# Performance work log

Hardware: AMD Instinct MI355X
Metric: run time of the kernel (lower is better)

The kernel has to match this reference:

```python
import jax, jax.numpy as jnp
import numpy as np

VOCAB, EMBED, HID, MAXLEN, BATCH = 32000, 512, 512, 64, 32
DEC_H = 2 * HID  # decoder hidden width = 2*hidden_size


def _lstm_cell(x, h, c, wx, wh, b):
    # PyTorch LSTMCell gate order: i, f, g, o
    gates = x @ wx + h @ wh + b
    i, f, g, o = jnp.split(gates, 4, axis=-1)
    c = jax.nn.sigmoid(f) * c + jax.nn.sigmoid(i) * jnp.tanh(g)
    h = jax.nn.sigmoid(o) * jnp.tanh(c)
    return h, c


def setup_inputs() -> dict:
    key = jax.random.key(0)
    ks = jax.random.split(key, 12)
    s = 0.02
    inp = {
        "x": jax.random.randint(ks[0], (BATCH, MAXLEN), 0, VOCAB),
        # encoder: embedding [V, E], LSTM cell E -> 2H
        "enc_embed": jax.random.normal(ks[1], (VOCAB, EMBED), jnp.float32) * s,
        "enc_wx": jax.random.normal(ks[2], (EMBED, 4 * DEC_H), jnp.float32) * s,
        "enc_wh": jax.random.normal(ks[3], (DEC_H, 4 * DEC_H), jnp.float32) * s,
        "enc_b": jnp.zeros((4 * DEC_H,), jnp.float32),
        # decoder: embedding [V, 2H], Bahdanau attn, combine, LSTM cell 2H -> 2H, out proj
        "dec_embed": jax.random.normal(ks[4], (VOCAB, DEC_H), jnp.float32) * s,
        "attn_w": jax.random.normal(ks[5], (2 * DEC_H, MAXLEN), jnp.float32) * s,
        "attn_b": jnp.zeros((MAXLEN,), jnp.float32),
        "comb_w": jax.random.normal(ks[6], (2 * DEC_H, DEC_H), jnp.float32) * s,
        "comb_b": jnp.zeros((DEC_H,), jnp.float32),
        "dec_wx": jax.random.normal(ks[7], (DEC_H, 4 * DEC_H), jnp.float32) * s,
        "dec_wh": jax.random.normal(ks[8], (DEC_H, 4 * DEC_H), jnp.float32) * s,
        "dec_b": jnp.zeros((4 * DEC_H,), jnp.float32),
        "out_w": jax.random.normal(ks[9], (DEC_H, VOCAB), jnp.float32) * s,
        "out_b": jnp.zeros((VOCAB,), jnp.float32),
    }
    return inp


def reference(x, enc_embed, enc_wx, enc_wh, enc_b, dec_embed, attn_w, attn_b,
              comb_w, comb_b, dec_wx, dec_wh, dec_b, out_w, out_b):
    B = x.shape[0]

    # ---- encoder: one token per step, scan over time ----
    def enc_step(carry, tok):
        h, c = carry
        e = enc_embed[tok]  # (B, E)
        h, c = _lstm_cell(e, h, c, enc_wx, enc_wh, enc_b)
        return (h, c), h

    h0 = jnp.zeros((B, DEC_H), jnp.float32)
    (_, _), enc_outs = jax.lax.scan(enc_step, (h0, h0), x.T)  # (L, B, 2H)
    enc_outs = enc_outs.transpose(1, 0, 2)  # (B, L, 2H)

    # ---- decoder: Bahdanau attention + greedy feedback, scan over steps ----
    def dec_step(carry, _):
        h, c, tok = carry
        e = dec_embed[tok]  # (B, 2H)
        aw = jax.nn.softmax(jnp.concatenate([e, h], -1) @ attn_w + attn_b, -1)  # (B, L)
        ctx = jnp.einsum('bl,bld->bd', aw, enc_outs)  # (B, 2H)
        inp = jax.nn.relu(jnp.concatenate([e, ctx], -1) @ comb_w + comb_b)
        h, c = _lstm_cell(inp, h, c, dec_wx, dec_wh, dec_b)
        logp = jax.nn.log_softmax(h @ out_w + out_b, -1)  # (B, V)
        tok = jnp.argmax(logp, -1)
        return (h, c, tok), logp

    tok0 = jnp.full((B,), 127, dtype=x.dtype)
    (_, _, _), outs = jax.lax.scan(dec_step, (h0, h0, tok0), None, length=MAXLEN)
    return outs.transpose(1, 0, 2)  # (B, L, V)
```

## Files before the change

kernel.cpp:

```cpp
#include <hip/hip_runtime.h>

#define B   32
#define L   64
#define DH  1024
#define G4  4096
#define EK  512
#define V   32000

__device__ __forceinline__ float sigm(float x){ return 1.f/(1.f+expf(-x)); }
__device__ __forceinline__ unsigned mono(float f){
  unsigned u = __float_as_uint(f);
  return (u & 0x80000000u) ? ~u : (u | 0x80000000u);
}

__global__ __launch_bounds__(256) void init_kernel(float* h, float* c){
  int i = blockIdx.x*256 + threadIdx.x;
  if (i < B*DH){ h[i]=0.f; c[i]=0.f; }
}

__global__ __launch_bounds__(256) void gates_kernel(
    int mode, int t,
    const int* __restrict__ x, const float* __restrict__ embed,
    const float* __restrict__ src1, int K1,
    const float* __restrict__ wx, const float* __restrict__ wh,
    const float* __restrict__ bias,
    const float* __restrict__ h_in, float* __restrict__ h_out,
    float* __restrict__ cst, float* __restrict__ enc_outs)
{
  __shared__ float es[128][36];
  __shared__ int tok_s[B];
  __shared__ float gate_s[4][8][B];
  int tid = threadIdx.x;
  int hc = tid & 7, g = (tid>>3)&3, rg = tid>>5;
  int jh = blockIdx.x*8 + hc;
  int jg = g*DH + jh;
  float a0=0.f,a1=0.f,a2=0.f,a3=0.f;
  if (mode==0 && tid < B) tok_s[tid] = x[tid*L + t];
  __syncthreads();
  for (int phase=0; phase<2; ++phase){
    int K = phase ? DH : K1;
    const float* W = phase ? wh : wx;
    for (int kb=0; kb<K; kb+=128){
      for (int i=0;i<16;++i){
        int idx = i*256 + tid;
        int b = idx >> 7, kk = idx & 127;
        int k = kb + kk;
        float v;
        if (phase)          v = h_in[b*DH + k];
        else if (mode==0)   v = embed[(long)tok_s[b]*EK + k];
        else { v = src1[b*DH + k]; v = v>0.f ? v : 0.f; }
        es[kk][b] = v;
      }
      __syncthreads();
      #pragma unroll 8
      for (int kk=0; kk<128; ++kk){
        float w = W[(long)(kb+kk)*G4 + jg];
        float4 hv = *reinterpret_cast<const float4*>(&es[kk][rg*4]);
        a0 += hv.x*w; a1 += hv.y*w; a2 += hv.z*w; a3 += hv.w*w;
      }
      __syncthreads();
    }
  }
  float bj = bias[jg];
  gate_s[g][hc][rg*4+0] = a0+bj;
  gate_s[g][hc][rg*4+1] = a1+bj;
  gate_s[g][hc][rg*4+2] = a2+bj;
  gate_s[g][hc][rg*4+3] = a3+bj;
  __syncthreads();
  if (tid < 64){
    int hc2 = tid & 7, rg2 = tid >> 3;
    int j = blockIdx.x*8 + hc2;
    for (int i=0;i<4;++i){
      int b = rg2*4 + i;
      float iv = gate_s[0][hc2][b];
      float fv = gate_s[1][hc2][b];
      float gv = gate_s[2][hc2][b];
      float ov = gate_s[3][hc2][b];
      float cn = sigm(fv)*cst[b*DH + j] + sigm(iv)*tanhf(gv);
      cst[b*DH + j] = cn;
      float hv = sigm(ov)*tanhf(cn);
      h_out[b*DH + j] = hv;
      if (enc_outs) enc_outs[((long)b*L + t)*DH + j] = hv;
    }
  }
}

__global__ __launch_bounds__(256) void attn_kernel(
    int t, const unsigned long long* __restrict__ ptok,
    const float* __restrict__ dec_embed, const float* __restrict__ attn_w,
    const float* __restrict__ attn_b, const float* __restrict__ h_in,
    const float* __restrict__ enc_outs,
    float* __restrict__ e_buf, float* __restrict__ ctx,
    float* __restrict__ inp, const float* __restrict__ comb_b)
{
  __shared__ float e_s[DH], h_s[DH], sc_s[4][64], aw_s[64];
  __shared__ int tok_sh;
  int b = blockIdx.x, tid = threadIdx.x;
  if (tid==0){
    int tok = 127;
    if (t > 0) tok = (int)(~(unsigned)(ptok[(t-1)*B + b] & 0xffffffffull));
    tok_sh = tok;
  }
  __syncthreads();
  int tok = tok_sh;
  for (int i=0;i<4;++i){
    int k = i*256 + tid;
    float ev = dec_embed[(long)tok*DH + k];
    float hv = h_in[b*DH + k];
    e_s[k]=ev; h_s[k]=hv;
    e_buf[b*DH + k] = ev;
    inp[b*DH + k] = comb_b[k];
  }
  __syncthreads();
  int l = tid & 63, ks = tid >> 6;
  float p = 0.f;
  for (int kk=0; kk<512; ++kk){
    int k = ks*512 + kk;
    float sv = (k < DH) ? e_s[k] : h_s[k-DH];
    p += sv * attn_w[(long)k*64 + l];
  }
  sc_s[ks][l] = p;
  __syncthreads();
  if (tid < 64){
    float s = sc_s[0][l]+sc_s[1][l]+sc_s[2][l]+sc_s[3][l] + attn_b[l];
    float m = s;
    for (int off=32; off; off>>=1) m = fmaxf(m, __shfl_xor(m, off));
    float e = expf(s-m);
    float sum = e;
    for (int off=32; off; off>>=1) sum += __shfl_xor(sum, off);
    aw_s[l] = e/sum;
  }
  __syncthreads();
  float c0=0.f,c1=0.f,c2=0.f,c3=0.f;
  for (int ll=0; ll<64; ++ll){
    float a = aw_s[ll];
    const float* er = &enc_outs[((long)b*L + ll)*DH];
    c0 += a*er[tid]; c1 += a*er[256+tid]; c2 += a*er[512+tid]; c3 += a*er[768+tid];
  }
  ctx[b*DH + tid]       = c0;
  ctx[b*DH + 256 + tid] = c1;
  ctx[b*DH + 512 + tid] = c2;
  ctx[b*DH + 768 + tid] = c3;
}

__global__ __launch_bounds__(256) void comb_kernel(
    const float* __restrict__ e_buf, const float* __restrict__ ctx,
    const float* __restrict__ comb_w, float* __restrict__ inp)
{
  __shared__ float es[128][36];
  int tid = threadIdx.x;
  int col = tid & 31, rg = tid >> 5;
  int j = blockIdx.x*32 + col;
  int kr = blockIdx.y;
  const float* src = (kr < 2) ? e_buf : ctx;
  int kbase0 = (kr & 1)*512;
  float a0=0.f,a1=0.f,a2=0.f,a3=0.f;
  for (int kb=0; kb<512; kb+=128){
    for (int i=0;i<16;++i){
      int idx = i*256 + tid;
      int b = idx >> 7, kk = idx & 127;
      es[kk][b] = src[b*DH + kbase0 + kb + kk];
    }
    __syncthreads();
    #pragma unroll 8
    for (int kk=0; kk<128; ++kk){
      float w = comb_w[(long)(kr*512 + kb + kk)*DH + j];
      float4 hv = *reinterpret_cast<const float4*>(&es[kk][rg*4]);
      a0 += hv.x*w; a1 += hv.y*w; a2 += hv.z*w; a3 += hv.w*w;
    }
    __syncthreads();
  }
  atomicAdd(&inp[(rg*4+0)*DH + j], a0);
  atomicAdd(&inp[(rg*4+1)*DH + j], a1);
  atomicAdd(&inp[(rg*4+2)*DH + j], a2);
  atomicAdd(&inp[(rg*4+3)*DH + j], a3);
}

__global__ __launch_bounds__(256) void outproj_kernel(
    int t, const float* __restrict__ hsrc, const float* __restrict__ out_w,
    const float* __restrict__ out_b, float* __restrict__ out,
    float* __restrict__ psum, unsigned long long* __restrict__ pmax)
{
  __shared__ float hs[128][36];
  __shared__ float red_s[B][33];
  __shared__ unsigned long long pk_s[B][33];
  int tid = threadIdx.x;
  int col = tid & 31, rg = tid >> 5;
  int j = blockIdx.x*32 + col;
  float a0=0.f,a1=0.f,a2=0.f,a3=0.f;
  for (int kb=0; kb<DH; kb+=128){
    for (int i=0;i<16;++i){
      int idx = i*256 + tid;
      int b = idx >> 7, kk = idx & 127;
      hs[kk][b] = hsrc[b*DH + kb + kk];
    }
    __syncthreads();
    #pragma unroll 8
    for (int kk=0; kk<128; ++kk){
      float w = out_w[(long)(kb+kk)*V + j];
      float4 hv = *reinterpret_cast<const float4*>(&hs[kk][rg*4]);
      a0 += hv.x*w; a1 += hv.y*w; a2 += hv.z*w; a3 += hv.w*w;
    }
    __syncthreads();
  }
  float bj = out_b[j];
  float lg0=a0+bj, lg1=a1+bj, lg2=a2+bj, lg3=a3+bj;
  int r0 = rg*4;
  out[((long)(r0+0)*L + t)*V + j] = lg0;
  out[((long)(r0+1)*L + t)*V + j] = lg1;
  out[((long)(r0+2)*L + t)*V + j] = lg2;
  out[((long)(r0+3)*L + t)*V + j] = lg3;
  unsigned nj = ~(unsigned)j;
  red_s[r0+0][col] = expf(lg0);
  red_s[r0+1][col] = expf(lg1);
  red_s[r0+2][col] = expf(lg2);
  red_s[r0+3][col] = expf(lg3);
  pk_s[r0+0][col] = ((unsigned long long)mono(lg0)<<32) | nj;
  pk_s[r0+1][col] = ((unsigned long long)mono(lg1)<<32) | nj;
  pk_s[r0+2][col] = ((unsigned long long)mono(lg2)<<32) | nj;
  pk_s[r0+3][col] = ((unsigned long long)mono(lg3)<<32) | nj;
  __syncthreads();
  if (tid < B){
    float s = 0.f; unsigned long long mx = 0ull;
    for (int cc=0; cc<32; ++cc){
      s += red_s[tid][cc];
      unsigned long long v = pk_s[tid][cc];
      if (v > mx) mx = v;
    }
    psum[tid*1024 + blockIdx.x] = s;
    pmax[tid*1024 + blockIdx.x] = mx;
  }
}

__global__ __launch_bounds__(256) void reduce_kernel(
    int t, const float* __restrict__ psum, const unsigned long long* __restrict__ pmax,
    float* __restrict__ lse, unsigned long long* __restrict__ ptok)
{
  __shared__ float ss[256];
  __shared__ unsigned long long ms[256];
  int row = blockIdx.x, tid = threadIdx.x;
  float s = 0.f; unsigned long long mx = 0ull;
  for (int i=tid; i<1000; i+=256){
    s += psum[row*1024 + i];
    unsigned long long v = pmax[row*1024 + i];
    if (v > mx) mx = v;
  }
  ss[tid]=s; ms[tid]=mx;
  __syncthreads();
  for (int off=128; off; off>>=1){
    if (tid < off){
      ss[tid] += ss[tid+off];
      if (ms[tid+off] > ms[tid]) ms[tid] = ms[tid+off];
    }
    __syncthreads();
  }
  if (tid==0){
    lse[t*B + row] = logf(ss[0]);
    ptok[t*B + row] = ms[0];
  }
}

__global__ __launch_bounds__(256) void norm_kernel(
    int t, float* __restrict__ out, const float* __restrict__ lse)
{
  int v = blockIdx.x*256 + threadIdx.x;
  int b = blockIdx.y;
  out[((long)b*L + t)*V + v] -= lse[t*B + b];
}

extern "C" void kernel_launch(void* const* d_in, const int* in_sizes, int n_in,
                              void* d_out, int out_size, void* d_ws, size_t ws_size,
                              hipStream_t stream)
{
  const int*   x         = (const int*)  d_in[0];
  const float* enc_embed = (const float*)d_in[1];
  const float* enc_wx    = (const float*)d_in[2];
  const float* enc_wh    = (const float*)d_in[3];
  const float* enc_b     = (const float*)d_in[4];
  const float* dec_embed = (const float*)d_in[5];
  const float* attn_w    = (const float*)d_in[6];
  const float* attn_b    = (const float*)d_in[7];
  const float* comb_w    = (const float*)d_in[8];
  const float* comb_b    = (const float*)d_in[9];
  const float* dec_wx    = (const float*)d_in[10];
  const float* dec_wh    = (const float*)d_in[11];
  const float* dec_b     = (const float*)d_in[12];
  const float* out_w     = (const float*)d_in[13];
  const float* out_b     = (const float*)d_in[14];
  float* out = (float*)d_out;

  float* enc_outs = (float*)d_ws;
  float* h0    = enc_outs + (size_t)B*L*DH;
  float* h1    = h0 + B*DH;
  float* c     = h1 + B*DH;
  float* e_buf = c  + B*DH;
  float* ctx   = e_buf + B*DH;
  float* inp   = ctx + B*DH;
  float* psum  = inp + B*DH;
  float* lse   = psum + B*1024;
  unsigned long long* pmax = (unsigned long long*)(lse + L*B);
  unsigned long long* ptok = pmax + B*1024;

  init_kernel<<<128,256,0,stream>>>(h0, c);
  for (int t=0; t<L; ++t){
    const float* hi = (t&1) ? h1 : h0;
    float*       ho = (t&1) ? h0 : h1;
    gates_kernel<<<128,256,0,stream>>>(0, t, x, enc_embed, nullptr, EK,
        enc_wx, enc_wh, enc_b, hi, ho, c, enc_outs);
  }
  init_kernel<<<128,256,0,stream>>>(h0, c);
  for (int t=0; t<L; ++t){
    const float* hi = (t&1) ? h1 : h0;
    float*       ho = (t&1) ? h0 : h1;
    attn_kernel<<<B,256,0,stream>>>(t, ptok, dec_embed, attn_w, attn_b,
        hi, enc_outs, e_buf, ctx, inp, comb_b);
    comb_kernel<<<dim3(32,4),256,0,stream>>>(e_buf, ctx, comb_w, inp);
    gates_kernel<<<128,256,0,stream>>>(1, t, nullptr, nullptr, inp, DH,
        dec_wx, dec_wh, dec_b, hi, ho, c, nullptr);
    outproj_kernel<<<1000,256,0,stream>>>(t, ho, out_w, out_b, out, psum, pmax);
    reduce_kernel<<<B,256,0,stream>>>(t, psum, pmax, lse, ptok);
    norm_kernel<<<dim3(125,B),256,0,stream>>>(t, out, lse);
  }
}
```

Measured before the change: 28.80 ms.

## Restructure LSTM decoder kernels around transposed activations and split-K gate GEMMs

Activations (embeddings, hidden state, context, combine input) are kept in a transposed [k][batch] layout so GEMM kernels read float4 activation vectors straight from global memory instead of staging them through shared memory. Gate GEMMs are split along K across grid.y, with partial sums written to a buffer that a separate cell kernel reduces before applying the LSTM nonlinearity. The output projection computes a 4x4 register tile per thread with 250 blocks. The per-step reduce kernel is removed: the argmax is folded into the next attention kernel, and log-softmax normalization is deferred to a single kernel after the loop. This adds launches for the cell kernel and needs more workspace, and the split-K partial buffer adds extra memory traffic.

```diff
diff --git a/kernel.cpp b/kernel.cpp
--- a/kernel.cpp
+++ b/kernel.cpp
@@ -7,109 +7,116 @@
 #define EK  512
 #define V   32000
 
+typedef unsigned long long ull;
+
 __device__ __forceinline__ float sigm(float x){ return 1.f/(1.f+expf(-x)); }
 __device__ __forceinline__ unsigned mono(float f){
   unsigned u = __float_as_uint(f);
   return (u & 0x80000000u) ? ~u : (u | 0x80000000u);
 }
 
-__global__ __launch_bounds__(256) void init_kernel(float* h, float* c){
+__global__ __launch_bounds__(256) void init_kernel(float* h, float* c, float* hT){
   int i = blockIdx.x*256 + threadIdx.x;
-  if (i < B*DH){ h[i]=0.f; c[i]=0.f; }
+  if (i < B*DH){ h[i]=0.f; c[i]=0.f; hT[i]=0.f; }
+}
+
+__global__ __launch_bounds__(256) void embT_kernel(const int* __restrict__ x,
+    const float* __restrict__ emb, float* __restrict__ encT){
+  int t = blockIdx.x;
+  int b = threadIdx.x & 31;
+  int k = blockIdx.y*8 + (threadIdx.x>>5);
+  int tok = x[b*L + t];
+  encT[((size_t)t*EK + k)*B + b] = emb[(size_t)tok*EK + k];
 }
 
 __global__ __launch_bounds__(256) void gates_kernel(
-    int mode, int t,
-    const int* __restrict__ x, const float* __restrict__ embed,
-    const float* __restrict__ src1, int K1,
+    const float* __restrict__ srcA, int krA, int relu_in,
+    const float* __restrict__ srcB,
     const float* __restrict__ wx, const float* __restrict__ wh,
-    const float* __restrict__ bias,
-    const float* __restrict__ h_in, float* __restrict__ h_out,
-    float* __restrict__ cst, float* __restrict__ enc_outs)
-{
-  __shared__ float es[128][36];
-  __shared__ int tok_s[B];
-  __shared__ float gate_s[4][8][B];
+    float* __restrict__ gpart)
+{
   int tid = threadIdx.x;
-  int hc = tid & 7, g = (tid>>3)&3, rg = tid>>5;
-  int jh = blockIdx.x*8 + hc;
-  int jg = g*DH + jh;
-  float a0=0.f,a1=0.f,a2=0.f,a3=0.f;
-  if (mode==0 && tid < B) tok_s[tid] = x[tid*L + t];
-  __syncthreads();
-  for (int phase=0; phase<2; ++phase){
-    int K = phase ? DH : K1;
-    const float* W = phase ? wh : wx;
-    for (int kb=0; kb<K; kb+=128){
-      for (int i=0;i<16;++i){
-        int idx = i*256 + tid;
-        int b = idx >> 7, kk = idx & 127;
-        int k = kb + kk;
-        float v;
-        if (phase)          v = h_in[b*DH + k];
-        else if (mode==0)   v = embed[(long)tok_s[b]*EK + k];
-        else { v = src1[b*DH + k]; v = v>0.f ? v : 0.f; }
-        es[kk][b] = v;
-      }
-      __syncthreads();
-      #pragma unroll 8
-      for (int kk=0; kk<128; ++kk){
-        float w = W[(long)(kb+kk)*G4 + jg];
-        float4 hv = *reinterpret_cast<const float4*>(&es[kk][rg*4]);
-        a0 += hv.x*w; a1 += hv.y*w; a2 += hv.z*w; a3 += hv.w*w;
-      }
-      __syncthreads();
+  int cp = tid & 31, rowq = tid >> 5;
+  int j = blockIdx.x*64 + cp*2;
+  int kr = blockIdx.y;
+  const float* src; const float* W; int relu = relu_in;
+  if (kr < krA){ src = srcA + (size_t)kr*512*B;        W = wx + (size_t)kr*512*G4; }
+  else         { src = srcB + (size_t)(kr-krA)*512*B;  W = wh + (size_t)(kr-krA)*512*G4; relu = 0; }
+  float a00=0,a01=0,a10=0,a11=0,a20=0,a21=0,a30=0,a31=0;
+  #pragma unroll 8
+  for (int kk=0; kk<512; ++kk){
+    float4 act = *reinterpret_cast<const float4*>(&src[kk*B + rowq*4]);
+    if (relu){
+      act.x = fmaxf(act.x,0.f); act.y = fmaxf(act.y,0.f);
+      act.z = fmaxf(act.z,0.f); act.w = fmaxf(act.w,0.f);
     }
-  }
-  float bj = bias[jg];
-  gate_s[g][hc][rg*4+0] = a0+bj;
-  gate_s[g][hc][rg*4+1] = a1+bj;
-  gate_s[g][hc][rg*4+2] = a2+bj;
-  gate_s[g][hc][rg*4+3] = a3+bj;
-  __syncthreads();
-  if (tid < 64){
-    int hc2 = tid & 7, rg2 = tid >> 3;
-    int j = blockIdx.x*8 + hc2;
-    for (int i=0;i<4;++i){
-      int b = rg2*4 + i;
-      float iv = gate_s[0][hc2][b];
-      float fv = gate_s[1][hc2][b];
-      float gv = gate_s[2][hc2][b];
-      float ov = gate_s[3][hc2][b];
-      float cn = sigm(fv)*cst[b*DH + j] + sigm(iv)*tanhf(gv);
-      cst[b*DH + j] = cn;
-      float hv = sigm(ov)*tanhf(cn);
-      h_out[b*DH + j] = hv;
-      if (enc_outs) enc_outs[((long)b*L + t)*DH + j] = hv;
-    }
-  }
+    float2 w = *reinterpret_cast<const float2*>(&W[(size_t)kk*G4 + j]);
+    a00 += act.x*w.x; a01 += act.x*w.y;
+    a10 += act.y*w.x; a11 += act.y*w.y;
+    a20 += act.z*w.x; a21 += act.z*w.y;
+    a30 += act.w*w.x; a31 += act.w*w.y;
+  }
+  *reinterpret_cast<float4*>(&gpart[((size_t)kr*G4 + j  )*B + rowq*4]) = make_float4(a00,a10,a20,a30);
+  *reinterpret_cast<float4*>(&gpart[((size_t)kr*G4 + j+1)*B + rowq*4]) = make_float4(a01,a11,a21,a31);
+}
+
+__global__ __launch_bounds__(256) void cell_kernel(
+    const float* __restrict__ gpart, int nkr,
+    const float* __restrict__ bias, float* __restrict__ c,
+    float* __restrict__ hT_out, float* __restrict__ h_out,
+    float* __restrict__ enc_outs, int t)
+{
+  int tid = threadIdx.x;
+  int b = tid & 31;
+  int j = blockIdx.x*8 + (tid>>5);
+  float iv = bias[j], fv = bias[DH+j], gv = bias[2*DH+j], ov = bias[3*DH+j];
+  for (int kr=0; kr<nkr; ++kr){
+    const float* g = &gpart[(size_t)kr*G4*B];
+    iv += g[((size_t)(0*DH+j))*B + b];
+    fv += g[((size_t)(1*DH+j))*B + b];
+    gv += g[((size_t)(2*DH+j))*B + b];
+    ov += g[((size_t)(3*DH+j))*B + b];
+  }
+  float cn = sigm(fv)*c[b*DH+j] + sigm(iv)*tanhf(gv);
+  c[b*DH+j] = cn;
+  float hv = sigm(ov)*tanhf(cn);
+  hT_out[j*B + b] = hv;
+  if (h_out)    h_out[b*DH + j] = hv;
+  if (enc_outs) enc_outs[((size_t)b*L + t)*DH + j] = hv;
 }
 
 __global__ __launch_bounds__(256) void attn_kernel(
-    int t, const unsigned long long* __restrict__ ptok,
+    int t, const ull* __restrict__ pmax,
     const float* __restrict__ dec_embed, const float* __restrict__ attn_w,
     const float* __restrict__ attn_b, const float* __restrict__ h_in,
     const float* __restrict__ enc_outs,
-    float* __restrict__ e_buf, float* __restrict__ ctx,
-    float* __restrict__ inp, const float* __restrict__ comb_b)
+    float* __restrict__ eT, float* __restrict__ ctxT,
+    float* __restrict__ inpT, const float* __restrict__ comb_b)
 {
   __shared__ float e_s[DH], h_s[DH], sc_s[4][64], aw_s[64];
+  __shared__ ull m_s[256];
   __shared__ int tok_sh;
   int b = blockIdx.x, tid = threadIdx.x;
-  if (tid==0){
-    int tok = 127;
-    if (t > 0) tok = (int)(~(unsigned)(ptok[(t-1)*B + b] & 0xffffffffull));
-    tok_sh = tok;
+  if (t > 0){
+    m_s[tid] = (tid < 250) ? pmax[b*256 + tid] : 0ull;
+    __syncthreads();
+    for (int off=128; off; off>>=1){
+      if (tid < off && m_s[tid+off] > m_s[tid]) m_s[tid] = m_s[tid+off];
+      __syncthreads();
+    }
+    if (tid==0) tok_sh = (int)(~(unsigned)(m_s[0] & 0xffffffffull));
+  } else {
+    if (tid==0) tok_sh = 127;
   }
   __syncthreads();
   int tok = tok_sh;
   for (int i=0;i<4;++i){
     int k = i*256 + tid;
-    float ev = dec_embed[(long)tok*DH + k];
+    float ev = dec_embed[(size_t)tok*DH + k];
     float hv = h_in[b*DH + k];
     e_s[k]=ev; h_s[k]=hv;
-    e_buf[b*DH + k] = ev;
-    inp[b*DH + k] = comb_b[k];
+    eT[k*B + b] = ev;
+    inpT[k*B + b] = comb_b[k];
   }
   __syncthreads();
   int l = tid & 63, ks = tid >> 6;
@@ -117,7 +124,7 @@
   for (int kk=0; kk<512; ++kk){
     int k = ks*512 + kk;
     float sv = (k < DH) ? e_s[k] : h_s[k-DH];
-    p += sv * attn_w[(long)k*64 + l];
+    p += sv * attn_w[(size_t)k*L + l];
   }
   sc_s[ks][l] = p;
   __syncthreads();
@@ -131,141 +138,111 @@
     aw_s[l] = e/sum;
   }
   __syncthreads();
-  float c0=0.f,c1=0.f,c2=0.f,c3=0.f;
+  float c0=0,c1=0,c2=0,c3=0;
   for (int ll=0; ll<64; ++ll){
     float a = aw_s[ll];
-    const float* er = &enc_outs[((long)b*L + ll)*DH];
+    const float* er = &enc_outs[((size_t)b*L + ll)*DH];
     c0 += a*er[tid]; c1 += a*er[256+tid]; c2 += a*er[512+tid]; c3 += a*er[768+tid];
   }
-  ctx[b*DH + tid]       = c0;
-  ctx[b*DH + 256 + tid] = c1;
-  ctx[b*DH + 512 + tid] = c2;
-  ctx[b*DH + 768 + tid] = c3;
+  ctxT[(      tid)*B + b] = c0;
+  ctxT[(256 + tid)*B + b] = c1;
+  ctxT[(512 + tid)*B + b] = c2;
+  ctxT[(768 + tid)*B + b] = c3;
 }
 
 __global__ __launch_bounds__(256) void comb_kernel(
-    const float* __restrict__ e_buf, const float* __restrict__ ctx,
-    const float* __restrict__ comb_w, float* __restrict__ inp)
-{
-  __shared__ float es[128][36];
+    const float* __restrict__ eT, const float* __restrict__ ctxT,
+    const float* __restrict__ comb_w, float* __restrict__ inpT)
+{
   int tid = threadIdx.x;
-  int col = tid & 31, rg = tid >> 5;
-  int j = blockIdx.x*32 + col;
+  int cp = tid & 31, rowq = tid >> 5;
+  int j = blockIdx.x*64 + cp*2;
   int kr = blockIdx.y;
-  const float* src = (kr < 2) ? e_buf : ctx;
-  int kbase0 = (kr & 1)*512;
-  float a0=0.f,a1=0.f,a2=0.f,a3=0.f;
-  for (int kb=0; kb<512; kb+=128){
-    for (int i=0;i<16;++i){
-      int idx = i*256 + tid;
-      int b = idx >> 7, kk = idx & 127;
-      es[kk][b] = src[b*DH + kbase0 + kb + kk];
+  const float* src = (kr < 2) ? (eT + (size_t)kr*512*B) : (ctxT + (size_t)(kr-2)*512*B);
+  const float* W = comb_w + (size_t)kr*512*DH;
+  float a00=0,a01=0,a10=0,a11=0,a20=0,a21=0,a30=0,a31=0;
+  #pragma unroll 8
+  for (int kk=0; kk<512; ++kk){
+    float4 act = *reinterpret_cast<const float4*>(&src[kk*B + rowq*4]);
+    float2 w = *reinterpret_cast<const float2*>(&W[(size_t)kk*DH + j]);
+    a00 += act.x*w.x; a01 += act.x*w.y;
+    a10 += act.y*w.x; a11 += act.y*w.y;
+    a20 += act.z*w.x; a21 += act.z*w.y;
+    a30 += act.w*w.x; a31 += act.w*w.y;
+  }
+  atomicAdd(&inpT[(size_t)(j  )*B + rowq*4+0], a00);
+  atomicAdd(&inpT[(size_t)(j  )*B + rowq*4+1], a10);
+  atomicAdd(&inpT[(size_t)(j  )*B + rowq*4+2], a20);
+  atomicAdd(&inpT[(size_t)(j  )*B + rowq*4+3], a30);
+  atomicAdd(&inpT[(size_t)(j+1)*B + rowq*4+0], a01);
+  atomicAdd(&inpT[(size_t)(j+1)*B + rowq*4+1], a11);
+  atomicAdd(&inpT[(size_t)(j+1)*B + rowq*4+2], a21);
+  atomicAdd(&inpT[(size_t)(j+1)*B + rowq*4+3], a31);
+}
+
+__global__ __launch_bounds__(256) void outproj_kernel(
+    int t, const float* __restrict__ hT, const float* __restrict__ out_w,
+    const float* __restrict__ out_b, float* __restrict__ out,
+    float* __restrict__ psum, ull* __restrict__ pmax)
+{
+  __shared__ float sred[B][33];
+  __shared__ ull   mred[B][33];
+  int tid = threadIdx.x;
+  int colq = tid & 31, rowq = tid >> 5;
+  int j0 = blockIdx.x*128 + colq*4;
+  int r0 = rowq*4;
+  float acc[4][4];
+  #pragma unroll
+  for (int r=0;r<4;++r){ acc[r][0]=0;acc[r][1]=0;acc[r][2]=0;acc[r][3]=0; }
+  #pragma unroll 8
+  for (int k=0;k<DH;++k){
+    float4 act = *reinterpret_cast<const float4*>(&hT[k*B + r0]);
+    float4 w   = *reinterpret_cast<const float4*>(&out_w[(size_t)k*V + j0]);
+    acc[0][0]+=act.x*w.x; acc[0][1]+=act.x*w.y; acc[0][2]+=act.x*w.z; acc[0][3]+=act.x*w.w;
+    acc[1][0]+=act.y*w.x; acc[1][1]+=act.y*w.y; acc[1][2]+=act.y*w.z; acc[1][3]+=act.y*w.w;
+    acc[2][0]+=act.z*w.x; acc[2][1]+=act.z*w.y; acc[2][2]+=act.z*w.z; acc[2][3]+=act.z*w.w;
+    acc[3][0]+=act.w*w.x; acc[3][1]+=act.w*w.y; acc[3][2]+=act.w*w.z; acc[3][3]+=act.w*w.w;
+  }
+  float4 bj = *reinterpret_cast<const float4*>(&out_b[j0]);
+  #pragma unroll
+  for (int r=0;r<4;++r){
+    float l0=acc[r][0]+bj.x, l1=acc[r][1]+bj.y, l2=acc[r][2]+bj.z, l3=acc[r][3]+bj.w;
+    *reinterpret_cast<float4*>(&out[((size_t)(r0+r)*L + t)*V + j0]) = make_float4(l0,l1,l2,l3);
+    float se = expf(l0)+expf(l1)+expf(l2)+expf(l3);
+    ull m0 = ((ull)mono(l0)<<32) | (unsigned)(~(unsigned)(j0  ));
+    ull m1 = ((ull)mono(l1)<<32) | (unsigned)(~(unsigned)(j0+1));
+    ull m2 = ((ull)mono(l2)<<32) | (unsigned)(~(unsigned)(j0+2));
+    ull m3 = ((ull)mono(l3)<<32) | (unsigned)(~(unsigned)(j0+3));
+    if (m1>m0) m0=m1; if (m3>m2) m2=m3; if (m2>m0) m0=m2;
+    sred[r0+r][colq] = se;
+    mred[r0+r][colq] = m0;
+  }
+  __syncthreads();
+  if (tid < B){
+    float s=0.f; ull mx=0ull;
+    for (int cc=0;cc<32;++cc){
+      s += sred[tid][cc];
+      if (mred[tid][cc] > mx) mx = mred[tid][cc];
     }
+    psum[((size_t)t*B + tid)*256 + blockIdx.x] = s;
+    pmax[tid*256 + blockIdx.x] = mx;
+  }
+}
+
+__global__ __launch_bounds__(256) void norm_kernel(
+    float* __restrict__ out, const float* __restrict__ psum)
+{
+  __shared__ float ss[256];
+  int t = blockIdx.x, b = blockIdx.y, tid = threadIdx.x;
+  ss[tid] = (tid < 250) ? psum[((size_t)t*B + b)*256 + tid] : 0.f;
+  __syncthreads();
+  for (int off=128; off; off>>=1){
+    if (tid < off) ss[tid] += ss[tid+off];
     __syncthreads();
-    #pragma unroll 8
-    for (int kk=0; kk<128; ++kk){
-      float w = comb_w[(long)(kr*512 + kb + kk)*DH + j];
-      float4 hv = *reinterpret_cast<const float4*>(&es[kk][rg*4]);
-      a0 += hv.x*w; a1 += hv.y*w; a2 += hv.z*w; a3 += hv.w*w;
-    }
-    __syncthreads();
-  }
-  atomicAdd(&inp[(rg*4+0)*DH + j], a0);
-  atomicAdd(&inp[(rg*4+1)*DH + j], a1);
-  atomicAdd(&inp[(rg*4+2)*DH + j], a2);
-  atomicAdd(&inp[(rg*4+3)*DH + j], a3);
-}
-
-__global__ __launch_bounds__(256) void outproj_kernel(
-    int t, const float* __restrict__ hsrc, const float* __restrict__ out_w,
-    const float* __restrict__ out_b, float* __restrict__ out,
-    float* __restrict__ psum, unsigned long long* __restrict__ pmax)
-{
-  __shared__ float hs[128][36];
-  __shared__ float red_s[B][33];
-  __shared__ unsigned long long pk_s[B][33];
-  int tid = threadIdx.x;
-  int col = tid & 31, rg = tid >> 5;
-  int j = blockIdx.x*32 + col;
-  float a0=0.f,a1=0.f,a2=0.f,a3=0.f;
-  for (int kb=0; kb<DH; kb+=128){
-    for (int i=0;i<16;++i){
-      int idx = i*256 + tid;
-      int b = idx >> 7, kk = idx & 127;
-      hs[kk][b] = hsrc[b*DH + kb + kk];
-    }
-    __syncthreads();
-    #pragma unroll 8
-    for (int kk=0; kk<128; ++kk){
-      float w = out_w[(long)(kb+kk)*V + j];
-      float4 hv = *reinterpret_cast<const float4*>(&hs[kk][rg*4]);
-      a0 += hv.x*w; a1 += hv.y*w; a2 += hv.z*w; a3 += hv.w*w;
-    }
-    __syncthreads();
-  }
-  float bj = out_b[j];
-  float lg0=a0+bj, lg1=a1+bj, lg2=a2+bj, lg3=a3+bj;
-  int r0 = rg*4;
-  out[((long)(r0+0)*L + t)*V + j] = lg0;
-  out[((long)(r0+1)*L + t)*V + j] = lg1;
-  out[((long)(r0+2)*L + t)*V + j] = lg2;
-  out[((long)(r0+3)*L + t)*V + j] = lg3;
-  unsigned nj = ~(unsigned)j;
-  red_s[r0+0][col] = expf(lg0);
-  red_s[r0+1][col] = expf(lg1);
-  red_s[r0+2][col] = expf(lg2);
-  red_s[r0+3][col] = expf(lg3);
-  pk_s[r0+0][col] = ((unsigned long long)mono(lg0)<<32) | nj;
-  pk_s[r0+1][col] = ((unsigned long long)mono(lg1)<<32) | nj;
-  pk_s[r0+2][col] = ((unsigned long long)mono(lg2)<<32) | nj;
-  pk_s[r0+3][col] = ((unsigned long long)mono(lg3)<<32) | nj;
-  __syncthreads();
-  if (tid < B){
-    float s = 0.f; unsigned long long mx = 0ull;
-    for (int cc=0; cc<32; ++cc){
-      s += red_s[tid][cc];
-      unsigned long long v = pk_s[tid][cc];
-      if (v > mx) mx = v;
-    }
-    psum[tid*1024 + blockIdx.x] = s;
-    pmax[tid*1024 + blockIdx.x] = mx;
-  }
-}
-
-__global__ __launch_bounds__(256) void reduce_kernel(
-    int t, const float* __restrict__ psum, const unsigned long long* __restrict__ pmax,
-    float* __restrict__ lse, unsigned long long* __restrict__ ptok)
-{
-  __shared__ float ss[256];
-  __shared__ unsigned long long ms[256];
-  int row = blockIdx.x, tid = threadIdx.x;
-  float s = 0.f; unsigned long long mx = 0ull;
-  for (int i=tid; i<1000; i+=256){
-    s += psum[row*1024 + i];
-    unsigned long long v = pmax[row*1024 + i];
-    if (v > mx) mx = v;
-  }
-  ss[tid]=s; ms[tid]=mx;
-  __syncthreads();
-  for (int off=128; off; off>>=1){
-    if (tid < off){
-      ss[tid] += ss[tid+off];
-      if (ms[tid+off] > ms[tid]) ms[tid] = ms[tid+off];
-    }
-    __syncthreads();
-  }
-  if (tid==0){
-    lse[t*B + row] = logf(ss[0]);
-    ptok[t*B + row] = ms[0];
-  }
-}
-
-__global__ __launch_bounds__(256) void norm_kernel(
-    int t, float* __restrict__ out, const float* __restrict__ lse)
-{
-  int v = blockIdx.x*256 + threadIdx.x;
-  int b = blockIdx.y;
-  out[((long)b*L + t)*V + v] -= lse[t*B + b];
+  }
+  float lse = logf(ss[0]);
+  size_t base = ((size_t)b*L + t)*V;
+  for (int i=tid; i<V; i+=256) out[base+i] -= lse;
 }
 
 extern "C" void kernel_launch(void* const* d_in, const int* in_sizes, int n_in,
@@ -289,36 +266,42 @@
   const float* out_b     = (const float*)d_in[14];
   float* out = (float*)d_out;
 
-  float* enc_outs = (float*)d_ws;
-  float* h0    = enc_outs + (size_t)B*L*DH;
-  float* h1    = h0 + B*DH;
-  float* c     = h1 + B*DH;
-  float* e_buf = c  + B*DH;
-  float* ctx   = e_buf + B*DH;
-  float* inp   = ctx + B*DH;
-  float* psum  = inp + B*DH;
-  float* lse   = psum + B*1024;
-  unsigned long long* pmax = (unsigned long long*)(lse + L*B);
-  unsigned long long* ptok = pmax + B*1024;
-
-  init_kernel<<<128,256,0,stream>>>(h0, c);
+  float* p = (float*)d_ws;
+  float* enc_outs = p;            p += (size_t)B*L*DH;
+  float* encT     = p;            p += (size_t)L*EK*B;
+  float* gpart    = p;            p += (size_t)4*G4*B;
+  float* psum     = p;            p += (size_t)L*B*256;
+  float* hT0      = p;            p += B*DH;
+  float* hT1      = p;            p += B*DH;
+  float* h0d      = p;            p += B*DH;
+  float* h1d      = p;            p += B*DH;
+  float* c        = p;            p += B*DH;
+  float* eT       = p;            p += B*DH;
+  float* ctxT     = p;            p += B*DH;
+  float* inpT     = p;            p += B*DH;
+  ull*   pmax     = (ull*)p;
+
+  init_kernel<<<128,256,0,stream>>>(h0d, c, hT0);
+  embT_kernel<<<dim3(L,64),256,0,stream>>>(x, enc_embed, encT);
   for (int t=0; t<L; ++t){
-    const float* hi = (t&1) ? h1 : h0;
-    float*       ho = (t&1) ? h0 : h1;
-    gates_kernel<<<128,256,0,stream>>>(0, t, x, enc_embed, nullptr, EK,
-        enc_wx, enc_wh, enc_b, hi, ho, c, enc_outs);
-  }
-  init_kernel<<<128,256,0,stream>>>(h0, c);
+    const float* hTi = (t&1) ? hT1 : hT0;
+    float*       hTo = (t&1) ? hT0 : hT1;
+    gates_kernel<<<dim3(64,3),256,0,stream>>>(encT + (size_t)t*EK*B, 1, 0,
+        hTi, enc_wx, enc_wh, gpart);
+    cell_kernel<<<128,256,0,stream>>>(gpart, 3, enc_b, c, hTo, nullptr, enc_outs, t);
+  }
+  init_kernel<<<128,256,0,stream>>>(h0d, c, hT0);
   for (int t=0; t<L; ++t){
-    const float* hi = (t&1) ? h1 : h0;
-    float*       ho = (t&1) ? h0 : h1;
-    attn_kernel<<<B,256,0,stream>>>(t, ptok, dec_embed, attn_w, attn_b,
-        hi, enc_outs, e_buf, ctx, inp, comb_b);
-    comb_kernel<<<dim3(32,4),256,0,stream>>>(e_buf, ctx, comb_w, inp);
-    gates_kernel<<<128,256,0,stream>>>(1, t, nullptr, nullptr, inp, DH,
-        dec_wx, dec_wh, dec_b, hi, ho, c, nullptr);
-    outproj_kernel<<<1000,256,0,stream>>>(t, ho, out_w, out_b, out, psum, pmax);
-    reduce_kernel<<<B,256,0,stream>>>(t, psum, pmax, lse, ptok);
-    norm_kernel<<<dim3(125,B),256,0,stream>>>(t, out, lse);
-  }
-}
+    const float* hTi = (t&1) ? hT1 : hT0;
+    float*       hTo = (t&1) ? hT0 : hT1;
+    const float* hi  = (t&1) ? h1d : h0d;
+    float*       ho  = (t&1) ? h0d : h1d;
+    attn_kernel<<<B,256,0,stream>>>(t, pmax, dec_embed, attn_w, attn_b,
+        hi, enc_outs, eT, ctxT, inpT, comb_b);
+    comb_kernel<<<dim3(16,4),256,0,stream>>>(eT, ctxT, comb_w, inpT);
+    gates_kernel<<<dim3(64,4),256,0,stream>>>(inpT, 2, 1, hTi, dec_wx, dec_wh, gpart);
+    cell_kernel<<<128,256,0,stream>>>(gpart, 4, dec_b, c, hTo, ho, nullptr, t);
+    outproj_kernel<<<250,256,0,stream>>>(t, hTo, out_w, out_b, out, psum, pmax);
+  }
+  norm_kernel<<<dim3(L,B),256,0,stream>>>(out, psum);
+}
```

Result: slower. 48.44 ms (+68.2%).
